# Optimization experiments

Hardware: AMD Instinct MI355X
Metric: run time of the kernel (lower is better)

The kernel has to match this reference:

```python
import jax, jax.numpy as jnp
import numpy as np

NUM_HEADS = 16
D_MODEL = 1024
HEAD_DIM = D_MODEL // NUM_HEADS
SCALE = float(np.sqrt(HEAD_DIM))  # NOTE: original multiplies q by sqrt(head_dim)
EPS = 1e-5


def layernorm(x, g, b):
    # LayerNorm over last dim (head_dim), learnable affine
    mu = jnp.mean(x, axis=-1, keepdims=True)
    var = jnp.mean(jnp.square(x - mu), axis=-1, keepdims=True)
    return (x - mu) * jax.lax.rsqrt(var + EPS) * g + b


def setup_inputs() -> dict:
    key = jax.random.key(0)
    ks = jax.random.split(key, 8)
    B, Nq, Nc = 2, 2048, 2048
    s = 0.02
    return {
        "x_query": jax.random.normal(ks[0], (B, Nq, D_MODEL), jnp.float32),
        "x_context": jax.random.normal(ks[1], (B, Nc, D_MODEL), jnp.float32),
        "Wq": jax.random.normal(ks[2], (D_MODEL, D_MODEL), jnp.float32) * s,
        "Wkv": jax.random.normal(ks[3], (D_MODEL, 2 * D_MODEL), jnp.float32) * s,
        "Wp": jax.random.normal(ks[4], (D_MODEL, D_MODEL), jnp.float32) * s,
        "bp": jnp.zeros((D_MODEL,), jnp.float32),
        "ln_g": jnp.ones((HEAD_DIM,), jnp.float32),
        "ln_b": jnp.zeros((HEAD_DIM,), jnp.float32),
    }


def reference(x_query, x_context, Wq, Wkv, Wp, bp, ln_g, ln_b):
    B, Nq, _ = x_query.shape
    Nc = x_context.shape[1]
    H, D = NUM_HEADS, HEAD_DIM
    # projections
    q = (x_query @ Wq).reshape(B, Nq, H, D).transpose(0, 2, 1, 3)  # b h n d
    kv = (x_context @ Wkv).reshape(B, Nc, 2, H, D)
    k = kv[:, :, 0].transpose(0, 2, 1, 3)  # b h n d
    v = kv[:, :, 1].transpose(0, 2, 1, 3)
    # QK-LayerNorm (shared params)
    q = layernorm(q, ln_g, ln_b)
    k = layernorm(k, ln_g, ln_b)
    # NOTE: faithful to source — q is MULTIPLIED by sqrt(head_dim)
    q = q * SCALE
    attn = jnp.einsum("bhqd,bhkd->bhqk", q, k)
    attn = jax.nn.softmax(attn, axis=-1)
    out = jnp.einsum("bhqk,bhkd->bhqd", attn, v)
    out = out.transpose(0, 2, 1, 3).reshape(B, Nq, H * D)
    return out @ Wp + bp
```

## Files before the change

### kernel.cpp

```cpp
#include <hip/hip_runtime.h>
#include <stdint.h>

#define NUM_HEADS 16
#define HEAD_DIM 64
#define D_MODEL 1024
#define SEQ 2048
#define BATCH 2

typedef unsigned short u16;
typedef _Float16 f16x8 __attribute__((ext_vector_type(8)));
typedef float f32x4 __attribute__((ext_vector_type(4)));

__device__ __forceinline__ u16 f2h(float f) {
    _Float16 h = (_Float16)f;
    return __builtin_bit_cast(u16, h);
}
__device__ __forceinline__ float h2f(u16 h) {
    return (float)__builtin_bit_cast(_Float16, h);
}
__device__ __forceinline__ uint32_t pkrtz(float a, float b) {
    return __builtin_bit_cast(uint32_t, __builtin_amdgcn_cvt_pkrtz(a, b));
}
__device__ __forceinline__ uint32_t pkrtn(float a, float b) {
    return (uint32_t)f2h(a) | ((uint32_t)f2h(b) << 16);
}

__device__ __forceinline__ float ex2(float x) {
#if __has_builtin(__builtin_amdgcn_exp2f)
    return __builtin_amdgcn_exp2f(x);
#else
    float r;
    asm("v_exp_f32 %0, %1" : "=v"(r) : "v"(x));
    return r;
#endif
}

__device__ __forceinline__ f16x8 ld8h(const u16* p) {
    return *reinterpret_cast<const f16x8*>(p);
}

__device__ __forceinline__ void gl_lds16(const void* g, void* l) {
    __builtin_amdgcn_global_load_lds(
        (const __attribute__((address_space(1))) void*)g,
        (__attribute__((address_space(3))) void*)l,
        16, 0, 0);
}

template <int CTRL>
__device__ __forceinline__ float dpp_mov(float x) {
    return __builtin_bit_cast(float,
        __builtin_amdgcn_update_dpp(0, __builtin_bit_cast(int, x), CTRL, 0xf, 0xf, true));
}
__device__ __forceinline__ float rowsum16(float x) {
    x += dpp_mov<0x121>(x);
    x += dpp_mov<0x122>(x);
    x += dpp_mov<0x124>(x);
    x += dpp_mov<0x128>(x);
    return x;
}

__global__ __launch_bounds__(256) void k_prep(const float* __restrict__ xq,
                                              const float* __restrict__ xc,
                                              const float* __restrict__ Wq,
                                              const float* __restrict__ Wkv,
                                              const float* __restrict__ Wp,
                                              u16* __restrict__ xq16,
                                              u16* __restrict__ xc16,
                                              u16* __restrict__ WqT16,
                                              u16* __restrict__ WkvT16,
                                              u16* __restrict__ WpT16) {
    __shared__ float tile[32][33];
    const int t = blockIdx.x;
    if (t < 8192) {
        int i = t * 256 + threadIdx.x;
        const float* src; u16* dst; int j;
        if (i < 1048576) { src = xq; dst = xq16; j = i; }
        else             { src = xc; dst = xc16; j = i - 1048576; }
        float4 v = reinterpret_cast<const float4*>(src)[j];
        ushort4 o;
        o.x = f2h(v.x); o.y = f2h(v.y); o.z = f2h(v.z); o.w = f2h(v.w);
        reinterpret_cast<ushort4*>(dst)[j] = o;
        return;
    }
    const float* W; u16* WT; int N, bi;
    if (t < 9216)       { W = Wq;  WT = WqT16;  N = 1024; bi = t - 8192; }
    else if (t < 11264) { W = Wkv; WT = WkvT16; N = 2048; bi = t - 9216; }
    else                { W = Wp;  WT = WpT16;  N = 1024; bi = t - 11264; }
    const int K = 1024;
    const int nb = N / 32;
    const int bn = (bi % nb) * 32, bk = (bi / nb) * 32;
    const int tx = threadIdx.x & 31;
    const int ty = threadIdx.x >> 5;
#pragma unroll
    for (int i = 0; i < 32; i += 8)
        tile[ty + i][tx] = W[(size_t)(bk + ty + i) * N + bn + tx];
    __syncthreads();
#pragma unroll
    for (int i = 0; i < 32; i += 8)
        WT[(size_t)(bn + ty + i) * K + bk + tx] = f2h(tile[tx][ty + i]);
}

__device__ __forceinline__ void gemm_mainloop_f16(const u16* __restrict__ A,
                                                  const u16* __restrict__ Bt,
                                                  u16* As, u16* Bs,
                                                  int tileM, int tileN, int K,
                                                  f32x4 acc[4][4]) {
    const int tid = threadIdx.x;
    const int lane = tid & 63;
    const int wv = tid >> 6;
    const int wm = wv >> 1, wn = wv & 1;
    const int quad = lane >> 4, l15 = lane & 15;

    const int c0 = tid, c1 = tid + 256;
    const u16* Ap0 = A + (size_t)(tileM + (c0 >> 2)) * K + (c0 & 3) * 8;
    const u16* Ap1 = A + (size_t)(tileM + (c1 >> 2)) * K + (c1 & 3) * 8;
    const u16* Bp0 = Bt + (size_t)(tileN + (c0 >> 2)) * K + (c0 & 3) * 8;
    const u16* Bp1 = Bt + (size_t)(tileN + (c1 >> 2)) * K + (c1 & 3) * 8;

    gl_lds16(Ap0, &As[c0 * 8]);
    gl_lds16(Ap1, &As[c1 * 8]);
    gl_lds16(Bp0, &Bs[c0 * 8]);
    gl_lds16(Bp1, &Bs[c1 * 8]);

    for (int k0 = 0; k0 < K; k0 += 32) {
        __syncthreads();
        const int cb = (k0 >> 5) & 1;
        if (k0 + 32 < K) {
            const int nbuf = cb ^ 1;
            gl_lds16(Ap0 + k0 + 32, &As[nbuf * 4096 + c0 * 8]);
            gl_lds16(Ap1 + k0 + 32, &As[nbuf * 4096 + c1 * 8]);
            gl_lds16(Bp0 + k0 + 32, &Bs[nbuf * 4096 + c0 * 8]);
            gl_lds16(Bp1 + k0 + 32, &Bs[nbuf * 4096 + c1 * 8]);
        }
        const int cbo = cb * 4096;
        f16x8 af[4], bfr[4];
#pragma unroll
        for (int mi = 0; mi < 4; ++mi)
            af[mi] = ld8h(&As[cbo + (wm * 64 + mi * 16 + l15) * 32 + quad * 8]);
#pragma unroll
        for (int ni = 0; ni < 4; ++ni)
            bfr[ni] = ld8h(&Bs[cbo + (wn * 64 + ni * 16 + l15) * 32 + quad * 8]);
#pragma unroll
        for (int mi = 0; mi < 4; ++mi)
#pragma unroll
            for (int ni = 0; ni < 4; ++ni)
                acc[mi][ni] = __builtin_amdgcn_mfma_f32_16x16x32_f16(
                    af[mi], bfr[ni], acc[mi][ni], 0, 0, 0);
    }
}

#define ACC_INIT()                                                   \
    f32x4 acc[4][4];                                                 \
    _Pragma("unroll") for (int i = 0; i < 4; ++i)                    \
        _Pragma("unroll") for (int j = 0; j < 4; ++j)                \
            acc[i][j] = (f32x4){0.f, 0.f, 0.f, 0.f};

__global__ __launch_bounds__(256, 2) void k_proj_f16(const u16* __restrict__ xq16,
                                                     const u16* __restrict__ xc16,
                                                     const u16* __restrict__ WqT16,
                                                     const u16* __restrict__ WkvT16,
                                                     const float* __restrict__ lng,
                                                     const float* __restrict__ lnb,
                                                     u16* __restrict__ Qh_h,
                                                     u16* __restrict__ Qh_l,
                                                     u16* __restrict__ Kh,
                                                     u16* __restrict__ VT) {
    __shared__ __align__(16) u16 As[2 * 128 * 32];
    __shared__ __align__(16) u16 Bs[2 * 128 * 32];
    const int bx = blockIdx.x;
    const int tileM = blockIdx.y * 128;
    const int tid = threadIdx.x;
    const int lane = tid & 63;
    const int wv = tid >> 6;
    const int wm = wv >> 1, wn = wv & 1;
    const int quad = lane >> 4, l15 = lane & 15;
    ACC_INIT();

    if (bx < 16) {
        const bool isQ = bx < 8;
        const int tileN = (bx & 7) * 128;
        const u16* Axx = isQ ? xq16 : xc16;
        const u16* Bt  = isQ ? WqT16 : WkvT16;
        const float scl = isQ ? 11.5415603294809528f : 1.0f;

        gemm_mainloop_f16(Axx, Bt, As, Bs, tileM, tileN, D_MODEL, acc);

        float gv[4], bv[4];
#pragma unroll
        for (int ni = 0; ni < 4; ++ni) { gv[ni] = lng[ni * 16 + l15]; bv[ni] = lnb[ni * 16 + l15]; }

#pragma unroll
        for (int mi = 0; mi < 4; ++mi) {
#pragma unroll
            for (int r = 0; r < 4; ++r) {
                float sum = 0.f, sq = 0.f;
#pragma unroll
                for (int ni = 0; ni < 4; ++ni) { float x = acc[mi][ni][r]; sum += x; sq += x * x; }
                sum = rowsum16(sum);
                sq  = rowsum16(sq);
                float mu = sum * (1.f / 64.f);
                float var = sq * (1.f / 64.f) - mu * mu;
                float rs = rsqrtf(var + 1e-5f);
                int m = tileM + wm * 64 + mi * 16 + quad * 4 + r;
                int bb = m >> 11, n = m & (SEQ - 1);
#pragma unroll
                for (int ni = 0; ni < 4; ++ni) {
                    int colg = tileN + wn * 64 + ni * 16 + l15;
                    int h = colg >> 6;
                    float y = ((acc[mi][ni][r] - mu) * rs * gv[ni] + bv[ni]) * scl;
                    size_t idx = (((size_t)bb * NUM_HEADS + h) * SEQ + n) * HEAD_DIM + (colg & 63);
                    u16 yh = f2h(y);
                    if (isQ) {
                        Qh_h[idx] = yh;
                        Qh_l[idx] = f2h(y - h2f(yh));
                    } else {
                        Kh[idx] = yh;
                    }
                }
            }
        }
    } else {
        const int tileN = D_MODEL + (bx - 16) * 128;
        gemm_mainloop_f16(xc16, WkvT16, As, Bs, tileM, tileN, D_MODEL, acc);
#pragma unroll
        for (int mi = 0; mi < 4; ++mi) {
            int m0 = tileM + wm * 64 + mi * 16 + quad * 4;
            int bb = m0 >> 11, n0 = m0 & (SEQ - 1);
#pragma unroll
            for (int ni = 0; ni < 4; ++ni) {
                int colg = tileN + wn * 64 + ni * 16 + l15 - D_MODEL;
                int h = colg >> 6, d = colg & 63;
                ushort4 o;
                o.x = f2h(acc[mi][ni][0]);
                o.y = f2h(acc[mi][ni][1]);
                o.z = f2h(acc[mi][ni][2]);
                o.w = f2h(acc[mi][ni][3]);
                *reinterpret_cast<ushort4*>(
                    &VT[(((size_t)bb * NUM_HEADS + h) * HEAD_DIM + d) * SEQ + n0]) = o;
            }
        }
    }
}

__global__ __launch_bounds__(256, 2) void k_gemm_out(const u16* __restrict__ A,
                                                     const u16* __restrict__ Bt,
                                                     const float* __restrict__ bp,
                                                     float* __restrict__ out) {
    __shared__ __align__(16) u16 As[2 * 128 * 32];
    __shared__ __align__(16) u16 Bs[2 * 128 * 32];
    const int tileM = blockIdx.y * 128, tileN = blockIdx.x * 128;
    const int tid = threadIdx.x;
    const int lane = tid & 63;
    const int wv = tid >> 6;
    const int wm = wv >> 1, wn = wv & 1;
    const int quad = lane >> 4, l15 = lane & 15;
    ACC_INIT();
    gemm_mainloop_f16(A, Bt, As, Bs, tileM, tileN, D_MODEL, acc);

    float bpv[4];
#pragma unroll
    for (int ni = 0; ni < 4; ++ni) bpv[ni] = bp[tileN + wn * 64 + ni * 16 + l15];
#pragma unroll
    for (int mi = 0; mi < 4; ++mi) {
#pragma unroll
        for (int r = 0; r < 4; ++r) {
            int m = tileM + wm * 64 + mi * 16 + quad * 4 + r;
#pragma unroll
            for (int ni = 0; ni < 4; ++ni) {
                int colg = tileN + wn * 64 + ni * 16 + l15;
                out[(size_t)m * D_MODEL + colg] = acc[mi][ni][r] + bpv[ni];
            }
        }
    }
}

__global__ __launch_bounds__(256) void k_attn(const u16* __restrict__ Qh_h,
                                              const u16* __restrict__ Qh_l,
                                              const u16* __restrict__ Kh,
                                              const u16* __restrict__ VT,
                                              u16* __restrict__ AO) {
    __shared__ __align__(16) u16 Ks[2 * 64 * 64];
    __shared__ __align__(16) u16 Vs[2 * 64 * 64];
    __shared__ __align__(16) u16 Ps[128 * 64];

    const int tid = threadIdx.x;
    const int lane = tid & 63;
    const int wv = tid >> 6;
    const int quad = lane >> 4, l15 = lane & 15;
    const int sw = l15 & 3;
    const int w1 = (l15 >> 2) & 1;
    const int id = blockIdx.x;
    const int bh = (id & 7) | (((id >> 7) & 3) << 3);
    const int qt = (id >> 3) & 15;

    const size_t bh_off = (size_t)bh * SEQ * HEAD_DIM;
    const u16* Vbh = VT + (size_t)bh * HEAD_DIM * SEQ;

    f16x8 qfh[2][2], qfl[2][2];
#pragma unroll
    for (int h = 0; h < 2; ++h)
#pragma unroll
        for (int kt = 0; kt < 2; ++kt) {
            size_t off = bh_off +
                (size_t)(qt * 128 + wv * 32 + h * 16 + l15) * HEAD_DIM + kt * 32 + quad * 8;
            qfh[h][kt] = ld8h(Qh_h + off);
            qfl[h][kt] = ld8h(Qh_l + off);
        }

    f16x8 ones;
#pragma unroll
    for (int i = 0; i < 8; ++i) ones[i] = (_Float16)1.0f;

    const int rr = lane >> 3;
    const int ss = lane & 7;
    const int cc = ss ^ rr;
    const int row0 = wv * 16 + rr;
    const u16* k0 = Kh + bh_off + (size_t)row0 * HEAD_DIM + cc * 8;
    const u16* v0 = Vbh + (size_t)row0 * SEQ + cc * 8;
    const int ldsW = (wv * 16) * 64;

    f32x4 acc_o[2][4];
    f32x4 acc_l0 = (f32x4){0.f, 0.f, 0.f, 0.f};
    f32x4 acc_l1 = (f32x4){0.f, 0.f, 0.f, 0.f};
    float m0 = -3.0e38f, m1 = -3.0e38f;
#pragma unroll
    for (int h = 0; h < 2; ++h)
#pragma unroll
        for (int ni = 0; ni < 4; ++ni) acc_o[h][ni] = (f32x4){0.f, 0.f, 0.f, 0.f};

    gl_lds16(k0,                &Ks[ldsW]);
    gl_lds16(k0 + 8 * HEAD_DIM, &Ks[ldsW + 8 * 64]);
    gl_lds16(v0,                &Vs[ldsW]);
    gl_lds16(v0 + 8 * SEQ,      &Vs[ldsW + 8 * 64]);

    const int psRow0 = (wv * 32 + l15) * 64;
    const int psRow1 = psRow0 + 16 * 64;
    const int psX = (quad ^ (w1 << 1)) * 4;

    for (int j = 0; j < SEQ / 64; ++j) {
        __syncthreads();
        if (j + 1 < SEQ / 64) {
            const int nb = (j + 1) & 1;
            const size_t ko = (size_t)(j + 1) * 64 * HEAD_DIM;
            const int vo = (j + 1) * 64;
            gl_lds16(k0 + ko,                &Ks[nb * 4096 + ldsW]);
            gl_lds16(k0 + ko + 8 * HEAD_DIM, &Ks[nb * 4096 + ldsW + 8 * 64]);
            gl_lds16(v0 + vo,                &Vs[nb * 4096 + ldsW]);
            gl_lds16(v0 + vo + 8 * SEQ,      &Vs[nb * 4096 + ldsW + 8 * 64]);
        }
        const int bb = (j & 1) * 4096;

        f32x4 s0[4], s1[4];
#pragma unroll
        for (int ni = 0; ni < 4; ++ni) {
            s0[ni] = (f32x4){0.f, 0.f, 0.f, 0.f};
            s1[ni] = (f32x4){0.f, 0.f, 0.f, 0.f};
        }
#pragma unroll
        for (int kt = 0; kt < 2; ++kt) {
            f16x8 kf[4];
#pragma unroll
            for (int ni = 0; ni < 4; ++ni) {
                int slot = (kt * 4 + quad) ^ (l15 & 7);
                kf[ni] = ld8h(&Ks[bb + (ni * 16 + l15) * 64 + slot * 8]);
            }
#pragma unroll
            for (int ni = 0; ni < 4; ++ni) {
                s0[ni] = __builtin_amdgcn_mfma_f32_16x16x32_f16(
                    kf[ni], qfh[0][kt], s0[ni], 0, 0, 0);
                s0[ni] = __builtin_amdgcn_mfma_f32_16x16x32_f16(
                    kf[ni], qfl[0][kt], s0[ni], 0, 0, 0);
                s1[ni] = __builtin_amdgcn_mfma_f32_16x16x32_f16(
                    kf[ni], qfh[1][kt], s1[ni], 0, 0, 0);
                s1[ni] = __builtin_amdgcn_mfma_f32_16x16x32_f16(
                    kf[ni], qfl[1][kt], s1[ni], 0, 0, 0);
            }
        }

        float mxa[2];
#pragma unroll
        for (int h = 0; h < 2; ++h) {
            const f32x4* sh = h ? s1 : s0;
            float a = fmaxf(fmaxf(sh[0][0], sh[0][1]), fmaxf(sh[0][2], sh[0][3]));
            float b = fmaxf(fmaxf(sh[1][0], sh[1][1]), fmaxf(sh[1][2], sh[1][3]));
            float c = fmaxf(fmaxf(sh[2][0], sh[2][1]), fmaxf(sh[2][2], sh[2][3]));
            float d = fmaxf(fmaxf(sh[3][0], sh[3][1]), fmaxf(sh[3][2], sh[3][3]));
            float mx = fmaxf(fmaxf(a, b), fmaxf(c, d));
            mx = fmaxf(mx, __shfl_xor(mx, 16, 64));
            mx = fmaxf(mx, __shfl_xor(mx, 32, 64));
            mxa[h] = mx;
        }
        float mnew0 = fmaxf(m0, mxa[0]);
        float mnew1 = fmaxf(m1, mxa[1]);
        if (__any(fmaxf(mxa[0] - m0, mxa[1] - m1) > 0.f)) {
            float a0 = ex2(m0 - mnew0);
            float a1 = ex2(m1 - mnew1);
#pragma unroll
            for (int ni = 0; ni < 4; ++ni) { acc_o[0][ni] *= a0; acc_o[1][ni] *= a1; }
            acc_l0[0] *= a0;
            acc_l1[0] *= a1;
            m0 = mnew0;
            m1 = mnew1;
        }
#pragma unroll
        for (int ni = 0; ni < 4; ++ni) {
            uint2 u;
            u.x = pkrtz(ex2(s0[ni][0] - mnew0), ex2(s0[ni][1] - mnew0));
            u.y = pkrtz(ex2(s0[ni][2] - mnew0), ex2(s0[ni][3] - mnew0));
            *reinterpret_cast<uint2*>(&Ps[psRow0 + psX + ((ni ^ sw) * 16)]) = u;
            uint2 v;
            v.x = pkrtz(ex2(s1[ni][0] - mnew1), ex2(s1[ni][1] - mnew1));
            v.y = pkrtz(ex2(s1[ni][2] - mnew1), ex2(s1[ni][3] - mnew1));
            *reinterpret_cast<uint2*>(&Ps[psRow1 + psX + ((ni ^ sw) * 16)]) = v;
        }

#pragma unroll
        for (int kt = 0; kt < 2; ++kt) {
            int pchunk = (kt * 2 + (quad >> 1)) ^ sw;
            int poff = pchunk * 16 + (((quad & 1) ^ w1) * 8);
            f16x8 pf0 = ld8h(&Ps[psRow0 + poff]);
            f16x8 pf1 = ld8h(&Ps[psRow1 + poff]);
            f16x8 vf[4];
#pragma unroll
            for (int ni = 0; ni < 4; ++ni) {
                int slot = (kt * 4 + quad) ^ (l15 & 7);
                vf[ni] = ld8h(&Vs[bb + (ni * 16 + l15) * 64 + slot * 8]);
            }
#pragma unroll
            for (int ni = 0; ni < 4; ++ni) {
                acc_o[0][ni] = __builtin_amdgcn_mfma_f32_16x16x32_f16(
                    vf[ni], pf0, acc_o[0][ni], 0, 0, 0);
                acc_o[1][ni] = __builtin_amdgcn_mfma_f32_16x16x32_f16(
                    vf[ni], pf1, acc_o[1][ni], 0, 0, 0);
            }
            acc_l0 = __builtin_amdgcn_mfma_f32_16x16x32_f16(ones, pf0, acc_l0, 0, 0, 0);
            acc_l1 = __builtin_amdgcn_mfma_f32_16x16x32_f16(ones, pf1, acc_l1, 0, 0, 0);
        }
    }

    const int b = bh >> 4, hh = bh & 15;
    const int echunk = quad ^ sw;
#pragma unroll
    for (int h = 0; h < 2; ++h) {
        const float inv = 1.0f / (h ? acc_l1[0] : acc_l0[0]);
        const int psRow = h ? psRow1 : psRow0;
        const f32x4* ao = acc_o[h];
#pragma unroll
        for (int ni = 0; ni < 4; ++ni) {
            uint2 u;
            u.x = pkrtn(ao[ni][0] * inv, ao[ni][1] * inv);
            u.y = pkrtn(ao[ni][2] * inv, ao[ni][3] * inv);
            *reinterpret_cast<uint2*>(&Ps[psRow + psX + ((ni ^ sw) * 16)]) = u;
        }
        const int qrow = qt * 128 + wv * 32 + h * 16 + l15;
        uint4 o0 = *reinterpret_cast<const uint4*>(&Ps[psRow + echunk * 16 + w1 * 8]);
        uint4 o1 = *reinterpret_cast<const uint4*>(&Ps[psRow + echunk * 16 + (1 - w1) * 8]);
        size_t outb = ((size_t)(b * SEQ + qrow)) * D_MODEL + hh * 64 + quad * 16;
        *reinterpret_cast<uint4*>(&AO[outb])     = o0;
        *reinterpret_cast<uint4*>(&AO[outb + 8]) = o1;
    }
}

extern "C" void kernel_launch(void* const* d_in, const int* in_sizes, int n_in,
                              void* d_out, int out_size, void* d_ws, size_t ws_size,
                              hipStream_t stream) {
    const float* xq  = (const float*)d_in[0];
    const float* xc  = (const float*)d_in[1];
    const float* Wq  = (const float*)d_in[2];
    const float* Wkv = (const float*)d_in[3];
    const float* Wp  = (const float*)d_in[4];
    const float* bp  = (const float*)d_in[5];
    const float* lng = (const float*)d_in[6];
    const float* lnb = (const float*)d_in[7];
    float* out = (float*)d_out;

    char* ws = (char*)d_ws;
    const size_t MB = 1 << 20;
    u16* xq16   = (u16*)(ws + 0 * MB);
    u16* xc16   = (u16*)(ws + 8 * MB);
    u16* WqT16  = (u16*)(ws + 16 * MB);
    u16* WkvT16 = (u16*)(ws + 18 * MB);
    u16* WpT16  = (u16*)(ws + 22 * MB);
    u16* Qh_h   = (u16*)(ws + 24 * MB);
    u16* Qh_l   = (u16*)(ws + 32 * MB);
    u16* Kh     = (u16*)(ws + 40 * MB);
    u16* VT     = (u16*)(ws + 48 * MB);
    u16* AO     = xq16;

    k_prep<<<12288, 256, 0, stream>>>(xq, xc, Wq, Wkv, Wp,
                                      xq16, xc16, WqT16, WkvT16, WpT16);
    k_proj_f16<<<dim3(24, 32), 256, 0, stream>>>(xq16, xc16, WqT16, WkvT16,
                                                 lng, lnb, Qh_h, Qh_l, Kh, VT);
    k_attn<<<512, 256, 0, stream>>>(Qh_h, Qh_l, Kh, VT, AO);
    k_gemm_out<<<dim3(8, 32), 256, 0, stream>>>(AO, WpT16, bp, out);
}
```

Measured before the change: 233.3 us.

## Stage QKV epilogue stores through LDS and halve attention P buffer for occupancy

The QKV projection epilogue now writes LayerNormed Q/K and transposed V tiles into shared memory and then emits coalesced 16-byte global stores, replacing scattered 2-byte and 8-byte writes. The attention kernel shrinks its P staging buffer to 64 rows by processing the two 16-row query halves one after another, and raises the launch-bounds occupancy hint to 4 blocks per CU. This trades extra LDS round trips and a serialized P path for better store coalescing and more resident waves. The end-of-kernel output staging reuses the smaller buffer per half within the same wave.

```diff
diff --git a/kernel.cpp b/kernel.cpp
--- a/kernel.cpp
+++ b/kernel.cpp
@@ -189,6 +189,13 @@
 #pragma unroll
         for (int ni = 0; ni < 4; ++ni) { gv[ni] = lng[ni * 16 + l15]; bv[ni] = lnb[ni * 16 + l15]; }
 
+        __syncthreads();
+        u16* reg = (wv < 2 ? As : Bs) + (wv & 1) * 4096;
+        const int h = (tileN + wn * 64) >> 6;
+        const int mbase0 = tileM + wm * 64;
+        const int bb = mbase0 >> 11;
+        const size_t gb0 = (((size_t)bb * NUM_HEADS + h) * SEQ + (mbase0 & (SEQ - 1))) * HEAD_DIM;
+
 #pragma unroll
         for (int mi = 0; mi < 4; ++mi) {
 #pragma unroll
@@ -201,43 +208,60 @@
                 float mu = sum * (1.f / 64.f);
                 float var = sq * (1.f / 64.f) - mu * mu;
                 float rs = rsqrtf(var + 1e-5f);
-                int m = tileM + wm * 64 + mi * 16 + quad * 4 + r;
-                int bb = m >> 11, n = m & (SEQ - 1);
+                const int wrow = quad * 4 + r;
 #pragma unroll
                 for (int ni = 0; ni < 4; ++ni) {
-                    int colg = tileN + wn * 64 + ni * 16 + l15;
-                    int h = colg >> 6;
                     float y = ((acc[mi][ni][r] - mu) * rs * gv[ni] + bv[ni]) * scl;
-                    size_t idx = (((size_t)bb * NUM_HEADS + h) * SEQ + n) * HEAD_DIM + (colg & 63);
                     u16 yh = f2h(y);
-                    if (isQ) {
-                        Qh_h[idx] = yh;
-                        Qh_l[idx] = f2h(y - h2f(yh));
-                    } else {
-                        Kh[idx] = yh;
-                    }
+                    reg[wrow * 64 + ni * 16 + l15] = yh;
+                    if (isQ) reg[1024 + wrow * 64 + ni * 16 + l15] = f2h(y - h2f(yh));
+                }
+            }
+            const size_t gmi = gb0 + (size_t)mi * 16 * 64;
+#pragma unroll
+            for (int p = 0; p < 2; ++p) {
+                const int row = p * 8 + (lane >> 3);
+                const int off = (lane & 7) * 8;
+                uint4 vh = *reinterpret_cast<const uint4*>(&reg[row * 64 + off]);
+                if (isQ) {
+                    uint4 vl = *reinterpret_cast<const uint4*>(&reg[1024 + row * 64 + off]);
+                    *reinterpret_cast<uint4*>(&Qh_h[gmi + row * 64 + off]) = vh;
+                    *reinterpret_cast<uint4*>(&Qh_l[gmi + row * 64 + off]) = vl;
+                } else {
+                    *reinterpret_cast<uint4*>(&Kh[gmi + row * 64 + off]) = vh;
                 }
             }
         }
     } else {
         const int tileN = D_MODEL + (bx - 16) * 128;
         gemm_mainloop_f16(xc16, WkvT16, As, Bs, tileM, tileN, D_MODEL, acc);
+
+        __syncthreads();
+        u16* reg = (wv < 2 ? As : Bs) + (wv & 1) * 4096;
 #pragma unroll
         for (int mi = 0; mi < 4; ++mi) {
-            int m0 = tileM + wm * 64 + mi * 16 + quad * 4;
-            int bb = m0 >> 11, n0 = m0 & (SEQ - 1);
 #pragma unroll
             for (int ni = 0; ni < 4; ++ni) {
-                int colg = tileN + wn * 64 + ni * 16 + l15 - D_MODEL;
-                int h = colg >> 6, d = colg & 63;
+                const int d = ni * 16 + l15;
+                const int pc = (mi * 2 + (quad >> 1)) ^ (d & 7);
                 ushort4 o;
                 o.x = f2h(acc[mi][ni][0]);
                 o.y = f2h(acc[mi][ni][1]);
                 o.z = f2h(acc[mi][ni][2]);
                 o.w = f2h(acc[mi][ni][3]);
-                *reinterpret_cast<ushort4*>(
-                    &VT[(((size_t)bb * NUM_HEADS + h) * HEAD_DIM + d) * SEQ + n0]) = o;
-            }
+                *reinterpret_cast<ushort4*>(&reg[d * 64 + pc * 8 + (quad & 1) * 4]) = o;
+            }
+        }
+        const int h = (tileN + wn * 64 - D_MODEL) >> 6;
+        const int m0 = tileM + wm * 64;
+        const int bb = m0 >> 11, n0 = m0 & (SEQ - 1);
+        const size_t vbase = (((size_t)bb * NUM_HEADS + h) * HEAD_DIM) * SEQ + n0;
+#pragma unroll
+        for (int p = 0; p < 8; ++p) {
+            const int d = p * 8 + (lane >> 3);
+            const int c = lane & 7;
+            uint4 v = *reinterpret_cast<const uint4*>(&reg[d * 64 + ((c ^ (d & 7)) * 8)]);
+            *reinterpret_cast<uint4*>(&VT[vbase + (size_t)d * SEQ + c * 8]) = v;
         }
     }
 }
@@ -274,14 +298,14 @@
     }
 }
 
-__global__ __launch_bounds__(256) void k_attn(const u16* __restrict__ Qh_h,
-                                              const u16* __restrict__ Qh_l,
-                                              const u16* __restrict__ Kh,
-                                              const u16* __restrict__ VT,
-                                              u16* __restrict__ AO) {
+__global__ __launch_bounds__(256, 4) void k_attn(const u16* __restrict__ Qh_h,
+                                                 const u16* __restrict__ Qh_l,
+                                                 const u16* __restrict__ Kh,
+                                                 const u16* __restrict__ VT,
+                                                 u16* __restrict__ AO) {
     __shared__ __align__(16) u16 Ks[2 * 64 * 64];
     __shared__ __align__(16) u16 Vs[2 * 64 * 64];
-    __shared__ __align__(16) u16 Ps[128 * 64];
+    __shared__ __align__(16) u16 Ps[64 * 64];
 
     const int tid = threadIdx.x;
     const int lane = tid & 63;
@@ -333,8 +357,7 @@
     gl_lds16(v0,                &Vs[ldsW]);
     gl_lds16(v0 + 8 * SEQ,      &Vs[ldsW + 8 * 64]);
 
-    const int psRow0 = (wv * 32 + l15) * 64;
-    const int psRow1 = psRow0 + 16 * 64;
+    const int psRow = (wv * 16 + l15) * 64;
     const int psX = (quad ^ (w1 << 1)) * 4;
 
     for (int j = 0; j < SEQ / 64; ++j) {
@@ -402,24 +425,19 @@
             m0 = mnew0;
             m1 = mnew1;
         }
+
 #pragma unroll
         for (int ni = 0; ni < 4; ++ni) {
             uint2 u;
             u.x = pkrtz(ex2(s0[ni][0] - mnew0), ex2(s0[ni][1] - mnew0));
             u.y = pkrtz(ex2(s0[ni][2] - mnew0), ex2(s0[ni][3] - mnew0));
-            *reinterpret_cast<uint2*>(&Ps[psRow0 + psX + ((ni ^ sw) * 16)]) = u;
-            uint2 v;
-            v.x = pkrtz(ex2(s1[ni][0] - mnew1), ex2(s1[ni][1] - mnew1));
-            v.y = pkrtz(ex2(s1[ni][2] - mnew1), ex2(s1[ni][3] - mnew1));
-            *reinterpret_cast<uint2*>(&Ps[psRow1 + psX + ((ni ^ sw) * 16)]) = v;
-        }
-
+            *reinterpret_cast<uint2*>(&Ps[psRow + psX + ((ni ^ sw) * 16)]) = u;
+        }
 #pragma unroll
         for (int kt = 0; kt < 2; ++kt) {
             int pchunk = (kt * 2 + (quad >> 1)) ^ sw;
             int poff = pchunk * 16 + (((quad & 1) ^ w1) * 8);
-            f16x8 pf0 = ld8h(&Ps[psRow0 + poff]);
-            f16x8 pf1 = ld8h(&Ps[psRow1 + poff]);
+            f16x8 pf = ld8h(&Ps[psRow + poff]);
             f16x8 vf[4];
 #pragma unroll
             for (int ni = 0; ni < 4; ++ni) {
@@ -427,14 +445,35 @@
                 vf[ni] = ld8h(&Vs[bb + (ni * 16 + l15) * 64 + slot * 8]);
             }
 #pragma unroll
+            for (int ni = 0; ni < 4; ++ni)
+                acc_o[0][ni] = __builtin_amdgcn_mfma_f32_16x16x32_f16(
+                    vf[ni], pf, acc_o[0][ni], 0, 0, 0);
+            acc_l0 = __builtin_amdgcn_mfma_f32_16x16x32_f16(ones, pf, acc_l0, 0, 0, 0);
+        }
+
+#pragma unroll
+        for (int ni = 0; ni < 4; ++ni) {
+            uint2 u;
+            u.x = pkrtz(ex2(s1[ni][0] - mnew1), ex2(s1[ni][1] - mnew1));
+            u.y = pkrtz(ex2(s1[ni][2] - mnew1), ex2(s1[ni][3] - mnew1));
+            *reinterpret_cast<uint2*>(&Ps[psRow + psX + ((ni ^ sw) * 16)]) = u;
+        }
+#pragma unroll
+        for (int kt = 0; kt < 2; ++kt) {
+            int pchunk = (kt * 2 + (quad >> 1)) ^ sw;
+            int poff = pchunk * 16 + (((quad & 1) ^ w1) * 8);
+            f16x8 pf = ld8h(&Ps[psRow + poff]);
+            f16x8 vf[4];
+#pragma unroll
             for (int ni = 0; ni < 4; ++ni) {
-                acc_o[0][ni] = __builtin_amdgcn_mfma_f32_16x16x32_f16(
-                    vf[ni], pf0, acc_o[0][ni], 0, 0, 0);
+                int slot = (kt * 4 + quad) ^ (l15 & 7);
+                vf[ni] = ld8h(&Vs[bb + (ni * 16 + l15) * 64 + slot * 8]);
+            }
+#pragma unroll
+            for (int ni = 0; ni < 4; ++ni)
                 acc_o[1][ni] = __builtin_amdgcn_mfma_f32_16x16x32_f16(
-                    vf[ni], pf1, acc_o[1][ni], 0, 0, 0);
-            }
-            acc_l0 = __builtin_amdgcn_mfma_f32_16x16x32_f16(ones, pf0, acc_l0, 0, 0, 0);
-            acc_l1 = __builtin_amdgcn_mfma_f32_16x16x32_f16(ones, pf1, acc_l1, 0, 0, 0);
+                    vf[ni], pf, acc_o[1][ni], 0, 0, 0);
+            acc_l1 = __builtin_amdgcn_mfma_f32_16x16x32_f16(ones, pf, acc_l1, 0, 0, 0);
         }
     }
 
@@ -443,7 +482,6 @@
 #pragma unroll
     for (int h = 0; h < 2; ++h) {
         const float inv = 1.0f / (h ? acc_l1[0] : acc_l0[0]);
-        const int psRow = h ? psRow1 : psRow0;
         const f32x4* ao = acc_o[h];
 #pragma unroll
         for (int ni = 0; ni < 4; ++ni) {
```

Result: slower. 269.6 us (+15.5%).
